# Performance work log

Hardware: AMD Instinct MI355X
Metric: run time of the kernel (lower is better)

The kernel has to match this reference:

```python
import jax, jax.numpy as jnp
import numpy as np
import math

# model / graph sizes
N_NODES, N_EDGES = 50000, 400000
IN_DIM, N_HID = 256, 128
NUM_TYPES, NUM_REL = 4, 5
N_HEADS, D_K = 4, 32
N_LAYERS, MAX_LEN = 2, 240
SQRT_DK = math.sqrt(D_K)


def _gelu(x):
    return jax.nn.gelu(x, approximate=False)  # torch F.gelu is exact erf


def _per_type_linear(x, types, W, b):
    # x:[n,din], types:[n] int, W:[T,din,dout], b:[T,dout]
    out = jnp.zeros((x.shape[0], W.shape[-1]), x.dtype)
    for t in range(W.shape[0]):  # small fixed type count
        out = jnp.where((types == t)[:, None], x @ W[t] + b[t], out)
    return out


def setup_inputs() -> dict:
    key = jax.random.key(0)
    ks = jax.random.split(key, 16)
    node_feature = jax.random.normal(ks[0], (N_NODES, IN_DIM), jnp.float32)
    node_type = jax.random.randint(ks[1], (N_NODES,), 0, NUM_TYPES)
    edge_index = jax.random.randint(ks[2], (2, N_EDGES), 0, N_NODES)
    edge_type = jax.random.randint(ks[3], (N_EDGES,), 0, NUM_REL)
    edge_time = jax.random.randint(ks[4], (N_EDGES,), 0, MAX_LEN)

    def w(k, shape, s=0.05):
        return jax.random.normal(k, shape, jnp.float32) * s

    adapt_W = w(ks[5], (NUM_TYPES, IN_DIM, N_HID))
    adapt_b = jnp.zeros((NUM_TYPES, N_HID), jnp.float32)
    Wk = w(ks[6], (N_LAYERS, NUM_TYPES, N_HID, N_HID))
    Wq = w(ks[7], (N_LAYERS, NUM_TYPES, N_HID, N_HID))
    Wv = w(ks[8], (N_LAYERS, NUM_TYPES, N_HID, N_HID))
    Wa = w(ks[9], (N_LAYERS, NUM_TYPES, N_HID, N_HID))
    bk = jnp.zeros((N_LAYERS, NUM_TYPES, N_HID), jnp.float32)
    bq = jnp.zeros((N_LAYERS, NUM_TYPES, N_HID), jnp.float32)
    bv = jnp.zeros((N_LAYERS, NUM_TYPES, N_HID), jnp.float32)
    ba = jnp.zeros((N_LAYERS, NUM_TYPES, N_HID), jnp.float32)
    rel_pri = jnp.ones((N_LAYERS, NUM_REL, N_HEADS), jnp.float32)
    rel_att = w(ks[10], (N_LAYERS, NUM_REL, N_HEADS, D_K, D_K), 0.1) + jnp.eye(D_K, dtype=jnp.float32)
    rel_msg = w(ks[11], (N_LAYERS, NUM_REL, N_HEADS, D_K, D_K), 0.1) + jnp.eye(D_K, dtype=jnp.float32)
    skip = jnp.ones((N_LAYERS, NUM_TYPES), jnp.float32)
    # fixed sinusoidal RTE table (pyHGT RelTemporalEncoding, requires_grad=False)
    pos = np.arange(MAX_LEN, dtype=np.float32)[:, None]
    div = np.exp(np.arange(0, N_HID, 2, dtype=np.float32) * -(math.log(10000.0) / N_HID))
    tab = np.zeros((MAX_LEN, N_HID), np.float32)
    tab[:, 0::2] = np.sin(pos * div) / math.sqrt(N_HID)
    tab[:, 1::2] = np.cos(pos * div) / math.sqrt(N_HID)
    rte_emb = jnp.asarray(tab)
    rte_W = w(ks[12], (N_LAYERS, N_HID, N_HID))
    rte_b = jnp.zeros((N_LAYERS, N_HID), jnp.float32)
    return dict(node_feature=node_feature, adapt_W=adapt_W, adapt_b=adapt_b,
                Wk=Wk, bk=bk, Wq=Wq, bq=bq, Wv=Wv, bv=bv, Wa=Wa, ba=ba,
                rel_pri=rel_pri, rel_att=rel_att, rel_msg=rel_msg, skip=skip,
                rte_emb=rte_emb, rte_W=rte_W, rte_b=rte_b,
                node_type=node_type, edge_index=edge_index,
                edge_type=edge_type, edge_time=edge_time)


def reference(node_feature, adapt_W, adapt_b, Wk, bk, Wq, bq, Wv, bv, Wa, ba,
              rel_pri, rel_att, rel_msg, skip, rte_emb, rte_W, rte_b,
              node_type, edge_index, edge_type, edge_time):
    n = node_feature.shape[0]
    src, dst = edge_index[0], edge_index[1]  # PyG: row0 = source j, row1 = target i
    st, tt = node_type[src], node_type[dst]
    # per-type input adaptation (all types use Linear + GELU)
    h = _gelu(_per_type_linear(node_feature, node_type, adapt_W, adapt_b))  # [N, n_hid]
    for l in range(N_LAYERS):  # HGTConv stack
        x_j, x_i = h[src], h[dst]
        s_e = x_j + rte_emb[edge_time] @ rte_W[l] + rte_b[l]  # RTE on source per edge
        k = _per_type_linear(s_e, st, Wk[l], bk[l]).reshape(-1, N_HEADS, D_K)
        v = _per_type_linear(s_e, st, Wv[l], bv[l]).reshape(-1, N_HEADS, D_K)
        q = _per_type_linear(x_i, tt, Wq[l], bq[l]).reshape(-1, N_HEADS, D_K)
        att = jnp.zeros((k.shape[0], N_HEADS), h.dtype)
        msg = jnp.zeros_like(v)
        for r in range(NUM_REL):  # small fixed relation count
            m = edge_type == r
            kr = jnp.einsum('ehd,hdk->ehk', k, rel_att[l, r])
            ar = jnp.einsum('ehd,ehd->eh', q, kr) * rel_pri[l, r] / SQRT_DK
            mr = jnp.einsum('ehd,hdk->ehk', v, rel_msg[l, r])
            att = jnp.where(m[:, None], ar, att)
            msg = jnp.where(m[:, None, None], mr, msg)
        # segment softmax over incoming edges of each target node
        amax = jax.lax.stop_gradient(jax.ops.segment_max(att, dst, num_segments=n))
        ex = jnp.exp(att - amax[dst])
        denom = jax.ops.segment_sum(ex, dst, num_segments=n)
        alpha = ex / (denom[dst] + 1e-16)
        aggr = jax.ops.segment_sum((msg * alpha[:, :, None]).reshape(-1, N_HEADS * D_K),
                                   dst, num_segments=n)  # [N, n_hid]
        g = _gelu(aggr)
        res = jnp.zeros_like(h)
        for t in range(NUM_TYPES):  # per-type output transform + gated skip
            a_t = jax.nn.sigmoid(skip[l, t])
            res = jnp.where((node_type == t)[:, None],
                            (g @ Wa[l, t] + ba[l, t]) * a_t + h * (1.0 - a_t), res)
        h = res
    return h
```

## Files before the change

### kernel.cpp

```cpp
#include <hip/hip_runtime.h>
#include <math.h>

#define NN     50000
#define NE     400000
#define INDIM  256
#define NH     128
#define NTYPE  4
#define NREL   5
#define NHEAD  4
#define DK     32
#define RSQRT_DK 0.17677669529663687f
#define BN     64
#define BN2    32
#define NSCAN_BLK ((NN + 255) / 256)
#define XB     260
#define XB2    132

__device__ __forceinline__ float gelu_f(float x){
    return 0.5f * x * (1.0f + erff(x * 0.70710678118654752f));
}

__global__ void GNN_nscatter(const int* __restrict__ ntype, int* __restrict__ ncur,
                             int* __restrict__ nperm){
    __shared__ int lcnt[4], lbase[4];
    int tid = threadIdx.x;
    if (tid < 4) lcnt[tid] = 0;
    __syncthreads();
    int n = blockIdx.x * 256 + tid;
    int t = 0, lpos = 0;
    bool ok = (n < NN);
    if (ok){ t = ntype[n]; lpos = atomicAdd(&lcnt[t], 1); }
    __syncthreads();
    if (tid < 4 && lcnt[tid] > 0) lbase[tid] = atomicAdd(&ncur[tid], lcnt[tid]);
    __syncthreads();
    if (ok) nperm[t * NN + lbase[t] + lpos] = n;
}

__global__ void GNN_deg(const int* __restrict__ edst, int* __restrict__ deg){
    int e = blockIdx.x * 256 + threadIdx.x;
    if (e < NE) atomicAdd(&deg[edst[e]], 1);
}

__global__ void GNN_scan1(const int* __restrict__ deg, int* __restrict__ rowptr,
                          int* __restrict__ bsum){
    __shared__ int s[256];
    int g = blockIdx.x * 256 + threadIdx.x;
    int v = (g < NN) ? deg[g] : 0;
    s[threadIdx.x] = v;
    __syncthreads();
    for (int off = 1; off < 256; off <<= 1){
        int t = (threadIdx.x >= off) ? s[threadIdx.x - off] : 0;
        __syncthreads();
        s[threadIdx.x] += t;
        __syncthreads();
    }
    if (g < NN) rowptr[g] = s[threadIdx.x] - v;
    if (threadIdx.x == 255) bsum[blockIdx.x] = s[255];
}

__global__ void GNN_scan2(const int* __restrict__ bsum, int* __restrict__ bbase){
    __shared__ int s[256];
    int v = (threadIdx.x < NSCAN_BLK) ? bsum[threadIdx.x] : 0;
    s[threadIdx.x] = v;
    __syncthreads();
    for (int off = 1; off < 256; off <<= 1){
        int t = (threadIdx.x >= off) ? s[threadIdx.x - off] : 0;
        __syncthreads();
        s[threadIdx.x] += t;
        __syncthreads();
    }
    bbase[threadIdx.x] = s[threadIdx.x] - v;
}

__global__ void GNN_scan3(int* __restrict__ rowptr, const int* __restrict__ bbase){
    int g = blockIdx.x * 256 + threadIdx.x;
    if (g < NN) rowptr[g] += bbase[blockIdx.x];
    if (g == 0) rowptr[NN] = NE;
}

__global__ void GNN_csr_scatter(const int* __restrict__ edst, const int* __restrict__ rowptr,
                                int* __restrict__ cursor, int* __restrict__ csr_e){
    int e = blockIdx.x * 256 + threadIdx.x;
    if (e >= NE) return;
    int d = edst[e];
    int pos = atomicAdd(&cursor[d], 1);
    csr_e[rowptr[d] + pos] = e;
}

template<int MODE>
__device__ __forceinline__ void gemm_tile(
    const float* __restrict__ X, int K,
    const float* __restrict__ W, const float* __restrict__ brow,
    float a_t, const float* __restrict__ Hprev,
    float* Xs, float* Ws, const int* nids,
    float* __restrict__ OUT)
{
    int tid = threadIdx.x;
    int cq = tid & 31, rq = tid >> 5;

    int xc0 = tid >> 6,          xr0i = tid & 63;
    int xc1 = (256 + tid) >> 6,  xr1i = tid & 63;
    int nid0 = nids[xr0i], nid1 = nids[xr1i];
    const float* xp0 = (nid0 >= 0) ? X + (size_t)nid0 * K + xc0 * 4 : nullptr;
    const float* xp1 = (nid1 >= 0) ? X + (size_t)nid1 * K + xc1 * 4 : nullptr;
    int wk = tid >> 5, wc4 = (tid & 31) * 4;

    float4 xr0, xr1, wr0, wr1, wr2, wr3;
    const float4 z4 = make_float4(0.f, 0.f, 0.f, 0.f);

    #define LOADREGS(k0)                                                        \
        xr0 = xp0 ? *(const float4*)(xp0 + (k0)) : z4;                          \
        xr1 = xp1 ? *(const float4*)(xp1 + (k0)) : z4;                          \
        wr0 = *(const float4*)(W + (size_t)((k0) + wk     ) * NH + wc4);        \
        wr1 = *(const float4*)(W + (size_t)((k0) + wk +  8) * NH + wc4);        \
        wr2 = *(const float4*)(W + (size_t)((k0) + wk + 16) * NH + wc4);        \
        wr3 = *(const float4*)(W + (size_t)((k0) + wk + 24) * NH + wc4);

    #define WRITELDS()                                                          \
        *(float4*)&Xs[xc0 * XB + xr0i * 4] = xr0;                               \
        *(float4*)&Xs[xc1 * XB + xr1i * 4] = xr1;                               \
        *(float4*)&Ws[(wk     ) * 128 + wc4] = wr0;                             \
        *(float4*)&Ws[(wk +  8) * 128 + wc4] = wr1;                             \
        *(float4*)&Ws[(wk + 16) * 128 + wc4] = wr2;                             \
        *(float4*)&Ws[(wk + 24) * 128 + wc4] = wr3;

    float acc[8][4];
    #pragma unroll
    for (int i = 0; i < 8; i++){ acc[i][0]=0.f; acc[i][1]=0.f; acc[i][2]=0.f; acc[i][3]=0.f; }

    LOADREGS(0);
    for (int k0 = 0; k0 < K; k0 += 32){
        WRITELDS();
        __syncthreads();
        if (k0 + 32 < K){ LOADREGS(k0 + 32); }
        #pragma unroll 2
        for (int c4 = 0; c4 < 8; c4++){
            float4 w0 = *(const float4*)&Ws[(c4*4+0)*128 + cq*4];
            float4 w1 = *(const float4*)&Ws[(c4*4+1)*128 + cq*4];
            float4 w2 = *(const float4*)&Ws[(c4*4+2)*128 + cq*4];
            float4 w3 = *(const float4*)&Ws[(c4*4+3)*128 + cq*4];
            #pragma unroll
            for (int i = 0; i < 8; i++){
                float4 xv = *(const float4*)&Xs[c4 * XB + (rq + 8*i) * 4];
                acc[i][0] += xv.x*w0.x + xv.y*w1.x + xv.z*w2.x + xv.w*w3.x;
                acc[i][1] += xv.x*w0.y + xv.y*w1.y + xv.z*w2.y + xv.w*w3.y;
                acc[i][2] += xv.x*w0.z + xv.y*w1.z + xv.z*w2.z + xv.w*w3.z;
                acc[i][3] += xv.x*w0.w + xv.y*w1.w + xv.z*w2.w + xv.w*w3.w;
            }
        }
        __syncthreads();
    }
    #undef LOADREGS
    #undef WRITELDS

    float4 b4 = *(const float4*)(brow + cq * 4);
    float one_m = 1.f - a_t;
    #pragma unroll
    for (int i = 0; i < 8; i++){
        int r = rq + 8*i;
        int nid = nids[r];
        if (nid < 0) continue;
        float v0 = acc[i][0] + b4.x, v1 = acc[i][1] + b4.y;
        float v2 = acc[i][2] + b4.z, v3 = acc[i][3] + b4.w;
        if (MODE == 0){ v0 = gelu_f(v0); v1 = gelu_f(v1); v2 = gelu_f(v2); v3 = gelu_f(v3); }
        if (MODE == 2){
            float4 hp = *(const float4*)(Hprev + (size_t)nid * NH + cq * 4);
            v0 = v0 * a_t + hp.x * one_m; v1 = v1 * a_t + hp.y * one_m;
            v2 = v2 * a_t + hp.z * one_m; v3 = v3 * a_t + hp.w * one_m;
        }
        *(float4*)(OUT + (size_t)nid * NH + cq * 4) = make_float4(v0, v1, v2, v3);
    }
}

template<int MODE>
__device__ __forceinline__ void gemm_tile32(
    const float* __restrict__ X, int K,
    const float* __restrict__ W, const float* __restrict__ brow,
    float a_t, const float* __restrict__ Hprev,
    float* Xs, float* Ws, const int* nids,
    float* __restrict__ OUT)
{
    int tid = threadIdx.x;
    int cq = tid & 31, rq = tid >> 5;

    int nid0 = nids[tid & 31];
    const float* xp0 = (nid0 >= 0) ? X + (size_t)nid0 * K + (tid >> 5) * 4 : nullptr;
    int wk = tid >> 5, wc4 = (tid & 31) * 4;
    int xdst = (tid >> 5) * XB2 + (tid & 31) * 4;

    float4 xr0, wr0, wr1, wr2, wr3;
    const float4 z4 = make_float4(0.f, 0.f, 0.f, 0.f);

    #define LOADREGS2(k0)                                                       \
        xr0 = xp0 ? *(const float4*)(xp0 + (k0)) : z4;                          \
        wr0 = *(const float4*)(W + (size_t)((k0) + wk     ) * NH + wc4);        \
        wr1 = *(const float4*)(W + (size_t)((k0) + wk +  8) * NH + wc4);        \
        wr2 = *(const float4*)(W + (size_t)((k0) + wk + 16) * NH + wc4);        \
        wr3 = *(const float4*)(W + (size_t)((k0) + wk + 24) * NH + wc4);

    #define WRITELDS2()                                                         \
        *(float4*)&Xs[xdst] = xr0;                                              \
        *(float4*)&Ws[(wk     ) * 128 + wc4] = wr0;                             \
        *(float4*)&Ws[(wk +  8) * 128 + wc4] = wr1;                             \
        *(float4*)&Ws[(wk + 16) * 128 + wc4] = wr2;                             \
        *(float4*)&Ws[(wk + 24) * 128 + wc4] = wr3;

    float acc[4][4];
    #pragma unroll
    for (int i = 0; i < 4; i++){ acc[i][0]=0.f; acc[i][1]=0.f; acc[i][2]=0.f; acc[i][3]=0.f; }

    LOADREGS2(0);
    for (int k0 = 0; k0 < K; k0 += 32){
        WRITELDS2();
        __syncthreads();
        if (k0 + 32 < K){ LOADREGS2(k0 + 32); }
        #pragma unroll 2
        for (int c4 = 0; c4 < 8; c4++){
            float4 w0 = *(const float4*)&Ws[(c4*4+0)*128 + cq*4];
            float4 w1 = *(const float4*)&Ws[(c4*4+1)*128 + cq*4];
            float4 w2 = *(const float4*)&Ws[(c4*4+2)*128 + cq*4];
            float4 w3 = *(const float4*)&Ws[(c4*4+3)*128 + cq*4];
            #pragma unroll
            for (int i = 0; i < 4; i++){
                float4 xv = *(const float4*)&Xs[c4 * XB2 + (rq + 8*i) * 4];
                acc[i][0] += xv.x*w0.x + xv.y*w1.x + xv.z*w2.x + xv.w*w3.x;
                acc[i][1] += xv.x*w0.y + xv.y*w1.y + xv.z*w2.y + xv.w*w3.y;
                acc[i][2] += xv.x*w0.z + xv.y*w1.z + xv.z*w2.z + xv.w*w3.z;
                acc[i][3] += xv.x*w0.w + xv.y*w1.w + xv.z*w2.w + xv.w*w3.w;
            }
        }
        __syncthreads();
    }
    #undef LOADREGS2
    #undef WRITELDS2

    float4 b4 = *(const float4*)(brow + cq * 4);
    float one_m = 1.f - a_t;
    #pragma unroll
    for (int i = 0; i < 4; i++){
        int r = rq + 8*i;
        int nid = nids[r];
        if (nid < 0) continue;
        float v0 = acc[i][0] + b4.x, v1 = acc[i][1] + b4.y;
        float v2 = acc[i][2] + b4.z, v3 = acc[i][3] + b4.w;
        if (MODE == 0){ v0 = gelu_f(v0); v1 = gelu_f(v1); v2 = gelu_f(v2); v3 = gelu_f(v3); }
        if (MODE == 2){
            float4 hp = *(const float4*)(Hprev + (size_t)nid * NH + cq * 4);
            v0 = v0 * a_t + hp.x * one_m; v1 = v1 * a_t + hp.y * one_m;
            v2 = v2 * a_t + hp.z * one_m; v3 = v3 * a_t + hp.w * one_m;
        }
        *(float4*)(OUT + (size_t)nid * NH + cq * 4) = make_float4(v0, v1, v2, v3);
    }
}

template<int MODE>
__global__ __launch_bounds__(256) void GNN_ptype_gemm(
    const float* __restrict__ X, int K,
    const float* __restrict__ Wall, const float* __restrict__ ball,
    const float* __restrict__ skiprow, const float* __restrict__ Hprev,
    const int* __restrict__ nperm, const int* __restrict__ counts,
    float* __restrict__ OUT)
{
    int t = blockIdx.y;
    int cnt = counts[t];
    int rbase = blockIdx.x * BN2;
    if (rbase >= cnt) return;
    __shared__ float Xs[8 * XB2];
    __shared__ float Ws[32 * 128];
    __shared__ int nids[BN2];
    int tid = threadIdx.x;
    if (tid < BN2){
        int idx = rbase + tid;
        nids[tid] = (idx < cnt) ? nperm[t * NN + idx] : -1;
    }
    __syncthreads();
    float a_t = 0.f;
    if (MODE == 2) a_t = 1.f / (1.f + expf(-skiprow[t]));
    gemm_tile32<MODE>(X, K, Wall + (size_t)t * K * NH, ball + t * NH,
                      a_t, Hprev, Xs, Ws, nids, OUT);
}

__global__ __launch_bounds__(256) void GNN_qkv_gemm(
    const float* __restrict__ X,
    const float* __restrict__ Wq, const float* __restrict__ bq,
    const float* __restrict__ Wk, const float* __restrict__ bk,
    const float* __restrict__ Wv, const float* __restrict__ bv,
    const int* __restrict__ nperm, const int* __restrict__ counts,
    float* __restrict__ Qn, float* __restrict__ Kn, float* __restrict__ Vn)
{
    int t = blockIdx.y;
    int cnt = counts[t];
    int rbase = blockIdx.x * BN;
    if (rbase >= cnt) return;
    __shared__ float Xs[8 * XB];
    __shared__ float Ws[32 * 128];
    __shared__ int nids[BN];
    int tid = threadIdx.x;
    if (tid < BN){
        int idx = rbase + tid;
        nids[tid] = (idx < cnt) ? nperm[t * NN + idx] : -1;
    }
    __syncthreads();
    int z = blockIdx.z;
    const float* W = (z == 0) ? Wq : (z == 1) ? Wk : Wv;
    const float* b = (z == 0) ? bq : (z == 1) ? bk : bv;
    float* OUT     = (z == 0) ? Qn : (z == 1) ? Kn : Vn;
    gemm_tile<1>(X, NH, W + (size_t)t * NH * NH, b + t * NH,
                 0.f, nullptr, Xs, Ws, nids, OUT);
}

__global__ void GNN_rte_tab(const float* __restrict__ rte_emb, const float* __restrict__ rW,
                            const float* __restrict__ rb, float* __restrict__ tab){
    int m = blockIdx.x, j = threadIdx.x;
    __shared__ float e[NH];
    e[j] = rte_emb[m * NH + j];
    __syncthreads();
    float a = rb[j];
    #pragma unroll 8
    for (int d = 0; d < NH; d++) a += e[d] * rW[d * NH + j];
    tab[m * NH + j] = a;
}

__global__ void GNN_rte_proj(const float* __restrict__ tab, const float* __restrict__ WkL,
                             const float* __restrict__ WvL, float* __restrict__ RK,
                             float* __restrict__ RV){
    int m = blockIdx.x, j = threadIdx.x;
    int sel = blockIdx.y; int t = sel >> 1; int which = sel & 1;
    const float* W = (which ? WvL : WkL) + (size_t)t * NH * NH;
    float* O = which ? RV : RK;
    __shared__ float e[NH];
    e[j] = tab[m * NH + j];
    __syncthreads();
    float a = 0.f;
    #pragma unroll 8
    for (int d = 0; d < NH; d++) a += e[d] * W[d * NH + j];
    O[(size_t)(t * 240 + m) * NH + j] = a;
}

__global__ __launch_bounds__(256) void GNN_qa(
    const float* __restrict__ Qn, const float* __restrict__ relA, float* __restrict__ QA)
{
    __shared__ float Atp[4 * 1072];
    int r = blockIdx.y;
    int nb = blockIdx.x * 64;
    int tid = threadIdx.x;
    const float* Ar = relA + (size_t)r * NHEAD * DK * DK;
    for (int x = tid; x < NHEAD * DK * DK; x += 256){
        int hh = x >> 10, rem = x & 1023, dd = rem >> 5, cc = rem & 31;
        Atp[hh * 1072 + (dd >> 2) * 132 + cc * 4 + (dd & 3)] = Ar[x];
    }
    __syncthreads();
    int cq = tid & 31, rq = tid >> 5;
    int h = cq >> 3;
    int abase = h * 1072 + (cq & 7) * 132;
    int rowoff[8];
    #pragma unroll
    for (int i = 0; i < 8; i++){
        int node = nb + rq + 8*i;
        if (node >= NN) node = NN - 1;
        rowoff[i] = node * NH + h * 32;
    }
    float acc[8][4];
    #pragma unroll
    for (int i = 0; i < 8; i++){ acc[i][0]=0.f; acc[i][1]=0.f; acc[i][2]=0.f; acc[i][3]=0.f; }
    #pragma unroll 2
    for (int c4 = 0; c4 < 8; c4++){
        float4 av0 = *(const float4*)&Atp[abase + c4 * 16 + 0];
        float4 av1 = *(const float4*)&Atp[abase + c4 * 16 + 4];
        float4 av2 = *(const float4*)&Atp[abase + c4 * 16 + 8];
        float4 av3 = *(const float4*)&Atp[abase + c4 * 16 + 12];
        #pragma unroll
        for (int i = 0; i < 8; i++){
            float4 qv = *(const float4*)(Qn + rowoff[i] + c4 * 4);
            acc[i][0] += qv.x*av0.x + qv.y*av1.x + qv.z*av2.x + qv.w*av3.x;
            acc[i][1] += qv.x*av0.y + qv.y*av1.y + qv.z*av2.y + qv.w*av3.y;
            acc[i][2] += qv.x*av0.z + qv.y*av1.z + qv.z*av2.z + qv.w*av3.z;
            acc[i][3] += qv.x*av0.w + qv.y*av1.w + qv.z*av2.w + qv.w*av3.w;
        }
    }
    #pragma unroll
    for (int i = 0; i < 8; i++){
        int node = nb + rq + 8*i;
        if (node >= NN) continue;
        *(float4*)(QA + ((size_t)r * NN + node) * NH + cq * 4) =
            make_float4(acc[i][0], acc[i][1], acc[i][2], acc[i][3]);
    }
}

__global__ __launch_bounds__(256) void GNN_edge_att(
    const float* __restrict__ Kn, const float* __restrict__ RK, const float* __restrict__ QA,
    const int* __restrict__ esrc, const int* __restrict__ edst,
    const int* __restrict__ etype, const int* __restrict__ etime,
    const int* __restrict__ ntype, const float* __restrict__ relP,
    float* __restrict__ att)
{
    int tid = threadIdx.x;
    int e = blockIdx.x * 8 + (tid >> 5);
    if (e >= NE) return;
    int lane = tid & 31;
    int s = esrc[e], d = edst[e], r = etype[e], tm = etime[e];
    int st = ntype[s];
    float4 k4 = *(const float4*)(Kn + (size_t)s * NH + lane * 4);
    float4 rk = *(const float4*)(RK + (size_t)(st * 240 + tm) * NH + lane * 4);
    float4 qa = *(const float4*)(QA + ((size_t)r * NN + d) * NH + lane * 4);
    float pv = (k4.x + rk.x) * qa.x + (k4.y + rk.y) * qa.y
             + (k4.z + rk.z) * qa.z + (k4.w + rk.w) * qa.w;
    pv += __shfl_xor(pv, 4);
    pv += __shfl_xor(pv, 2);
    pv += __shfl_xor(pv, 1);
    if ((lane & 7) == 0){
        int head = lane >> 3;
        att[(size_t)e * NHEAD + head] = pv * relP[r * NHEAD + head] * RSQRT_DK;
    }
}

__global__ __launch_bounds__(256) void GNN_node_aggr(
    const float* __restrict__ att, const float* __restrict__ Vn, const float* __restrict__ RV,
    const int* __restrict__ rowptr, const int* __restrict__ csr_e,
    const int* __restrict__ esrc, const int* __restrict__ etype,
    const int* __restrict__ etime, const int* __restrict__ ntype,
    float* __restrict__ P)
{
    int tid = threadIdx.x;
    int i = blockIdx.x * 8 + (tid >> 5);
    if (i >= NN) return;
    int lane = tid & 31;
    int head = lane >> 3;
    int beg = rowptr[i], end = rowptr[i + 1];
    float mx = -3.4e38f;
    for (int k = beg; k < end; k++){
        int e = csr_e[k];
        mx = fmaxf(mx, att[(size_t)e * NHEAD + head]);
    }
    float4 acc[NREL];
    #pragma unroll
    for (int rr = 0; rr < NREL; rr++) acc[rr] = make_float4(0.f, 0.f, 0.f, 0.f);
    float den = 0.f;
    for (int k = beg; k < end; k++){
        int e = csr_e[k];
        int s = esrc[e], r = etype[e], tm = etime[e];
        int st = ntype[s];
        float ex = expf(att[(size_t)e * NHEAD + head] - mx);
        den += ex;
        float4 v4 = *(const float4*)(Vn + (size_t)s * NH + lane * 4);
        float4 rv = *(const float4*)(RV + (size_t)(st * 240 + tm) * NH + lane * 4);
        float vx = v4.x + rv.x, vy = v4.y + rv.y, vz = v4.z + rv.z, vw = v4.w + rv.w;
        #pragma unroll
        for (int rr = 0; rr < NREL; rr++){
            float w = (rr == r) ? ex : 0.f;
            acc[rr].x += w * vx; acc[rr].y += w * vy;
            acc[rr].z += w * vz; acc[rr].w += w * vw;
        }
    }
    float inv = 1.f / (den + 1e-16f);
    #pragma unroll
    for (int rr = 0; rr < NREL; rr++){
        *(float4*)(P + ((size_t)rr * NN + i) * NH + lane * 4) =
            make_float4(acc[rr].x * inv, acc[rr].y * inv, acc[rr].z * inv, acc[rr].w * inv);
    }
}

__global__ __launch_bounds__(256) void GNN_pm(
    const float* __restrict__ P, const float* __restrict__ relM, float* __restrict__ aggr)
{
    __shared__ float Msp[2][4 * 1072];
    int tid = threadIdx.x;
    int nb = blockIdx.x * 64;
    int cq = tid & 31, rq = tid >> 5;
    int h = cq >> 3;
    int mbase = h * 1072 + (cq & 7) * 132;
    int rowoff[8];
    #pragma unroll
    for (int i = 0; i < 8; i++){
        int node = nb + rq + 8*i;
        if (node >= NN) node = NN - 1;
        rowoff[i] = node * NH + h * 32;
    }
    float acc[8][4];
    #pragma unroll
    for (int i = 0; i < 8; i++){ acc[i][0]=0.f; acc[i][1]=0.f; acc[i][2]=0.f; acc[i][3]=0.f; }

    #pragma unroll
    for (int j = 0; j < 4; j++){
        int s = tid + 256 * j;
        float4 mv = *(const float4*)(relM + 4 * s);
        *(float4*)&Msp[0][(s >> 8) * 1072 + (s & 7) * 132 + ((s >> 3) & 31) * 4] = mv;
    }
    __syncthreads();

    #pragma unroll
    for (int r = 0; r < NREL; r++){
        float4 mpre[4];
        if (r + 1 < NREL){
            const float* Mn = relM + (size_t)(r + 1) * NHEAD * DK * DK;
            #pragma unroll
            for (int j = 0; j < 4; j++)
                mpre[j] = *(const float4*)(Mn + 4 * (tid + 256 * j));
        }
        const float* Ms = Msp[r & 1];
        const float* Pr = P + (size_t)r * NN * NH;
        #pragma unroll 2
        for (int d4 = 0; d4 < 8; d4++){
            float4 mv0 = *(const float4*)&Ms[mbase + d4 * 16 + 0];
            float4 mv1 = *(const float4*)&Ms[mbase + d4 * 16 + 4];
            float4 mv2 = *(const float4*)&Ms[mbase + d4 * 16 + 8];
            float4 mv3 = *(const float4*)&Ms[mbase + d4 * 16 + 12];
            #pragma unroll
            for (int i = 0; i < 8; i++){
                float4 pv = *(const float4*)(Pr + rowoff[i] + d4 * 4);
                acc[i][0] += pv.x*mv0.x + pv.y*mv1.x + pv.z*mv2.x + pv.w*mv3.x;
                acc[i][1] += pv.x*mv0.y + pv.y*mv1.y + pv.z*mv2.y + pv.w*mv3.y;
                acc[i][2] += pv.x*mv0.z + pv.y*mv1.z + pv.z*mv2.z + pv.w*mv3.z;
                acc[i][3] += pv.x*mv0.w + pv.y*mv1.w + pv.z*mv2.w + pv.w*mv3.w;
            }
        }
        if (r + 1 < NREL){
            #pragma unroll
            for (int j = 0; j < 4; j++){
                int s = tid + 256 * j;
                *(float4*)&Msp[(r + 1) & 1][(s >> 8) * 1072 + (s & 7) * 132 +
                                            ((s >> 3) & 31) * 4] = mpre[j];
            }
            __syncthreads();
        }
    }
    #pragma unroll
    for (int i = 0; i < 8; i++){
        int node = nb + rq + 8*i;
        if (node >= NN) continue;
        *(float4*)(aggr + (size_t)node * NH + cq * 4) =
            make_float4(gelu_f(acc[i][0]), gelu_f(acc[i][1]),
                        gelu_f(acc[i][2]), gelu_f(acc[i][3]));
    }
}

extern "C" void kernel_launch(void* const* d_in, const int* in_sizes, int n_in,
                              void* d_out, int out_size, void* d_ws, size_t ws_size,
                              hipStream_t stream)
{
    const float* node_feature = (const float*)d_in[0];
    const float* adapt_W = (const float*)d_in[1];
    const float* adapt_b = (const float*)d_in[2];
    const float* Wk = (const float*)d_in[3];
    const float* bk = (const float*)d_in[4];
    const float* Wq = (const float*)d_in[5];
    const float* bq = (const float*)d_in[6];
    const float* Wv = (const float*)d_in[7];
    const float* bv = (const float*)d_in[8];
    const float* Wa = (const float*)d_in[9];
    const float* ba = (const float*)d_in[10];
    const float* rel_pri = (const float*)d_in[11];
    const float* rel_att = (const float*)d_in[12];
    const float* rel_msg = (const float*)d_in[13];
    const float* skip = (const float*)d_in[14];
    const float* rte_emb = (const float*)d_in[15];
    const float* rte_W = (const float*)d_in[16];
    const float* rte_b = (const float*)d_in[17];
    const int* node_type = (const int*)d_in[18];
    const int* edge_index = (const int*)d_in[19];
    const int* edge_type = (const int*)d_in[20];
    const int* edge_time = (const int*)d_in[21];
    const int* esrc = edge_index;
    const int* edst = edge_index + NE;

    char* p = (char*)d_ws;
    auto alloc = [&](size_t bytes) -> char* {
        char* r = p; p += (bytes + 255) & ~(size_t)255; return r;
    };
    float* hA    = (float*)alloc((size_t)NN * NH * 4);
    float* Qn    = (float*)alloc((size_t)NN * NH * 4);
    float* Kn    = (float*)alloc((size_t)NN * NH * 4);
    float* Vn    = (float*)alloc((size_t)NN * NH * 4);
    float* QA    = (float*)alloc((size_t)NREL * NN * NH * 4);
    float* rtab  = (float*)alloc((size_t)240 * NH * 4);
    float* RK    = (float*)alloc((size_t)NTYPE * 240 * NH * 4);
    float* RV    = (float*)alloc((size_t)NTYPE * 240 * NH * 4);
    int* nperm   = (int*)alloc((size_t)NTYPE * NN * 4);
    int* rowptr  = (int*)alloc((size_t)(NN + 1) * 4);
    int* csr_e   = (int*)alloc((size_t)NE * 4);
    int* deg     = (int*)alloc((size_t)2 * NN * 4);
    int* cursor  = deg + NN;
    int* bsum    = (int*)alloc(256 * 4);
    int* bbase   = (int*)alloc(256 * 4);
    int* ncur    = (int*)alloc(64);
    float* att   = Qn;
    float* Pbuf  = QA;
    float* aggr  = Kn;

    hipMemsetAsync(ncur, 0, 64, stream);
    hipMemsetAsync(deg, 0, (size_t)2 * NN * 4, stream);

    GNN_nscatter<<<(NN + 255) / 256, 256, 0, stream>>>(node_type, ncur, nperm);
    GNN_deg<<<(NE + 255) / 256, 256, 0, stream>>>(edst, deg);
    GNN_scan1<<<NSCAN_BLK, 256, 0, stream>>>(deg, rowptr, bsum);
    GNN_scan2<<<1, 256, 0, stream>>>(bsum, bbase);
    GNN_scan3<<<NSCAN_BLK, 256, 0, stream>>>(rowptr, bbase);
    GNN_csr_scatter<<<(NE + 255) / 256, 256, 0, stream>>>(edst, rowptr, cursor, csr_e);

    dim3 pgrid((NN + BN2 - 1) / BN2, NTYPE);
    dim3 qgrid((NN + BN - 1) / BN, NTYPE, 3);
    GNN_ptype_gemm<0><<<pgrid, 256, 0, stream>>>(node_feature, INDIM, adapt_W, adapt_b,
                                                 nullptr, nullptr, nperm, ncur, hA);
    const float* hin = hA;
    for (int l = 0; l < 2; l++){
        const float* WkL = Wk + (size_t)l * NTYPE * NH * NH;
        const float* WqL = Wq + (size_t)l * NTYPE * NH * NH;
        const float* WvL = Wv + (size_t)l * NTYPE * NH * NH;
        const float* WaL = Wa + (size_t)l * NTYPE * NH * NH;
        const float* bkL = bk + (size_t)l * NTYPE * NH;
        const float* bqL = bq + (size_t)l * NTYPE * NH;
        const float* bvL = bv + (size_t)l * NTYPE * NH;
        const float* baL = ba + (size_t)l * NTYPE * NH;
        const float* relA = rel_att + (size_t)l * NREL * NHEAD * DK * DK;
        const float* relM = rel_msg + (size_t)l * NREL * NHEAD * DK * DK;
        const float* relP = rel_pri + (size_t)l * NREL * NHEAD;

        GNN_rte_tab<<<240, 128, 0, stream>>>(rte_emb, rte_W + (size_t)l * NH * NH,
                                             rte_b + (size_t)l * NH, rtab);
        GNN_rte_proj<<<dim3(240, NTYPE * 2), 128, 0, stream>>>(rtab, WkL, WvL, RK, RV);

        GNN_qkv_gemm<<<qgrid, 256, 0, stream>>>(
            hin, WqL, bqL, WkL, bkL, WvL, bvL, nperm, ncur, Qn, Kn, Vn);

        GNN_qa<<<dim3((NN + 63) / 64, NREL), 256, 0, stream>>>(Qn, relA, QA);

        GNN_edge_att<<<(NE + 7) / 8, 256, 0, stream>>>(
            Kn, RK, QA, esrc, edst, edge_type, edge_time, node_type, relP, att);

        GNN_node_aggr<<<(NN + 7) / 8, 256, 0, stream>>>(
            att, Vn, RV, rowptr, csr_e, esrc, edge_type, edge_time, node_type, Pbuf);

        GNN_pm<<<(NN + 63) / 64, 256, 0, stream>>>(Pbuf, relM, aggr);

        float* hout = (l == 0) ? hA : (float*)d_out;
        GNN_ptype_gemm<2><<<pgrid, 256, 0, stream>>>(
            aggr, NH, WaL, baL, skip + (size_t)l * NTYPE, hin,
            nperm, ncur, hout);
        hin = hout;
    }
}
```

Baseline: 1.099 ms.

## Fuse per-relation message transform into node aggregation kernel

Drops the separate GNN_pm kernel. GNN_node_aggr now keeps each node's five per-relation aggregates in shared memory and applies rel_msg and GELU in place. This avoids writing and re-reading a 5×N×128 float intermediate buffer in global memory on every layer, and removes one launch per layer. In exchange, each wavefront reads the rel_msg matrices straight from global memory through the cache instead of a staged shared tile, and the aggregation kernel gains extra FMA work and shared-memory pressure.

```diff
diff --git a/kernel.cpp b/kernel.cpp
--- a/kernel.cpp
+++ b/kernel.cpp
@@ -419,10 +419,12 @@
     const int* __restrict__ rowptr, const int* __restrict__ csr_e,
     const int* __restrict__ esrc, const int* __restrict__ etype,
     const int* __restrict__ etime, const int* __restrict__ ntype,
-    float* __restrict__ P)
-{
-    int tid = threadIdx.x;
-    int i = blockIdx.x * 8 + (tid >> 5);
+    const float* __restrict__ relM, float* __restrict__ aggr)
+{
+    __shared__ float Ps[8 * 720];
+    int tid = threadIdx.x;
+    int nslot = tid >> 5;
+    int i = blockIdx.x * 8 + nslot;
     if (i >= NN) return;
     int lane = tid & 31;
     int head = lane >> 3;
@@ -453,85 +455,33 @@
         }
     }
     float inv = 1.f / (den + 1e-16f);
+    float* Pn = &Ps[nslot * 720];
+    int c4 = (lane & 7) * 4;
     #pragma unroll
     for (int rr = 0; rr < NREL; rr++){
-        *(float4*)(P + ((size_t)rr * NN + i) * NH + lane * 4) =
+        *(float4*)&Pn[rr * 144 + head * 36 + c4] =
             make_float4(acc[rr].x * inv, acc[rr].y * inv, acc[rr].z * inv, acc[rr].w * inv);
     }
-}
-
-__global__ __launch_bounds__(256) void GNN_pm(
-    const float* __restrict__ P, const float* __restrict__ relM, float* __restrict__ aggr)
-{
-    __shared__ float Msp[2][4 * 1072];
-    int tid = threadIdx.x;
-    int nb = blockIdx.x * 64;
-    int cq = tid & 31, rq = tid >> 5;
-    int h = cq >> 3;
-    int mbase = h * 1072 + (cq & 7) * 132;
-    int rowoff[8];
-    #pragma unroll
-    for (int i = 0; i < 8; i++){
-        int node = nb + rq + 8*i;
-        if (node >= NN) node = NN - 1;
-        rowoff[i] = node * NH + h * 32;
-    }
-    float acc[8][4];
-    #pragma unroll
-    for (int i = 0; i < 8; i++){ acc[i][0]=0.f; acc[i][1]=0.f; acc[i][2]=0.f; acc[i][3]=0.f; }
-
-    #pragma unroll
-    for (int j = 0; j < 4; j++){
-        int s = tid + 256 * j;
-        float4 mv = *(const float4*)(relM + 4 * s);
-        *(float4*)&Msp[0][(s >> 8) * 1072 + (s & 7) * 132 + ((s >> 3) & 31) * 4] = mv;
-    }
-    __syncthreads();
-
-    #pragma unroll
-    for (int r = 0; r < NREL; r++){
-        float4 mpre[4];
-        if (r + 1 < NREL){
-            const float* Mn = relM + (size_t)(r + 1) * NHEAD * DK * DK;
-            #pragma unroll
-            for (int j = 0; j < 4; j++)
-                mpre[j] = *(const float4*)(Mn + 4 * (tid + 256 * j));
-        }
-        const float* Ms = Msp[r & 1];
-        const float* Pr = P + (size_t)r * NN * NH;
+    float4 out = make_float4(0.f, 0.f, 0.f, 0.f);
+    #pragma unroll
+    for (int rr = 0; rr < NREL; rr++){
+        const float* Mr = relM + ((size_t)rr * NHEAD + head) * (DK * DK) + c4;
+        const float* Pr = &Pn[rr * 144 + head * 36];
         #pragma unroll 2
         for (int d4 = 0; d4 < 8; d4++){
-            float4 mv0 = *(const float4*)&Ms[mbase + d4 * 16 + 0];
-            float4 mv1 = *(const float4*)&Ms[mbase + d4 * 16 + 4];
-            float4 mv2 = *(const float4*)&Ms[mbase + d4 * 16 + 8];
-            float4 mv3 = *(const float4*)&Ms[mbase + d4 * 16 + 12];
-            #pragma unroll
-            for (int i = 0; i < 8; i++){
-                float4 pv = *(const float4*)(Pr + rowoff[i] + d4 * 4);
-                acc[i][0] += pv.x*mv0.x + pv.y*mv1.x + pv.z*mv2.x + pv.w*mv3.x;
-                acc[i][1] += pv.x*mv0.y + pv.y*mv1.y + pv.z*mv2.y + pv.w*mv3.y;
-                acc[i][2] += pv.x*mv0.z + pv.y*mv1.z + pv.z*mv2.z + pv.w*mv3.z;
-                acc[i][3] += pv.x*mv0.w + pv.y*mv1.w + pv.z*mv2.w + pv.w*mv3.w;
-            }
-        }
-        if (r + 1 < NREL){
-            #pragma unroll
-            for (int j = 0; j < 4; j++){
-                int s = tid + 256 * j;
-                *(float4*)&Msp[(r + 1) & 1][(s >> 8) * 1072 + (s & 7) * 132 +
-                                            ((s >> 3) & 31) * 4] = mpre[j];
-            }
-            __syncthreads();
-        }
-    }
-    #pragma unroll
-    for (int i = 0; i < 8; i++){
-        int node = nb + rq + 8*i;
-        if (node >= NN) continue;
-        *(float4*)(aggr + (size_t)node * NH + cq * 4) =
-            make_float4(gelu_f(acc[i][0]), gelu_f(acc[i][1]),
-                        gelu_f(acc[i][2]), gelu_f(acc[i][3]));
-    }
+            float4 pv = *(const float4*)(Pr + d4 * 4);
+            float4 m0 = *(const float4*)(Mr + (d4*4+0) * DK);
+            float4 m1 = *(const float4*)(Mr + (d4*4+1) * DK);
+            float4 m2 = *(const float4*)(Mr + (d4*4+2) * DK);
+            float4 m3 = *(const float4*)(Mr + (d4*4+3) * DK);
+            out.x += pv.x*m0.x + pv.y*m1.x + pv.z*m2.x + pv.w*m3.x;
+            out.y += pv.x*m0.y + pv.y*m1.y + pv.z*m2.y + pv.w*m3.y;
+            out.z += pv.x*m0.z + pv.y*m1.z + pv.z*m2.z + pv.w*m3.z;
+            out.w += pv.x*m0.w + pv.y*m1.w + pv.z*m2.w + pv.w*m3.w;
+        }
+    }
+    *(float4*)(aggr + (size_t)i * NH + lane * 4) =
+        make_float4(gelu_f(out.x), gelu_f(out.y), gelu_f(out.z), gelu_f(out.w));
 }
 
 extern "C" void kernel_launch(void* const* d_in, const int* in_sizes, int n_in,
@@ -584,7 +534,6 @@
     int* bbase   = (int*)alloc(256 * 4);
     int* ncur    = (int*)alloc(64);
     float* att   = Qn;
-    float* Pbuf  = QA;
     float* aggr  = Kn;
 
     hipMemsetAsync(ncur, 0, 64, stream);
@@ -628,9 +577,8 @@
             Kn, RK, QA, esrc, edst, edge_type, edge_time, node_type, relP, att);
 
         GNN_node_aggr<<<(NN + 7) / 8, 256, 0, stream>>>(
-            att, Vn, RV, rowptr, csr_e, esrc, edge_type, edge_time, node_type, Pbuf);
-
-        GNN_pm<<<(NN + 63) / 64, 256, 0, stream>>>(Pbuf, relM, aggr);
+            att, Vn, RV, rowptr, csr_e, esrc, edge_type, edge_time, node_type,
+            relM, aggr);
 
         float* hout = (l == 0) ? hA : (float*)d_out;
         GNN_ptype_gemm<2><<<pgrid, 256, 0, stream>>>(
```

New measurement: 1.182 ms. 1.08x slower.
